# Kernel tuning notes

Measured on AMD Instinct MI355X. Metric: run time of the kernel, lower is better.

## Reference

```python
import jax, jax.numpy as jnp
import numpy as np

EPS = 1e-10

def _log_scaling(feats):
    # feats: (N, 15) raw attributes
    lshape = jnp.sqrt(feats[:, 7:8]) / (jnp.sqrt(feats[:, 6:7]) + EPS)  # sqrt(pca_small)/sqrt(pca_big)
    cosangle = jnp.cos(feats[:, 5:6])
    sinangle = jnp.sin(feats[:, 5:6])
    logged = jnp.log(jnp.abs(feats[:, 5:]) + EPS)  # cols 5..14 logged
    # drop logged angle (col 5), keep logged cols 6..14
    return jnp.concatenate([feats[:, :5], logged[:, 1:], lshape, cosangle, sinangle], axis=1)  # (N,17)


def setup_inputs() -> dict:
    rng = np.random.RandomState(0)
    N = 2 ** 21          # number of maxtree components
    H = W = 4096         # image size
    # parent pointers: sorted tree, parent[i] < i; root (node 0) marked -1
    parent = (rng.rand(N) * np.maximum(np.arange(N), 1)).astype(np.int32)
    parent[0] = -1
    # per-node gray-level increment w.r.t. parent
    diff = rng.randn(N).astype(np.float32)
    # raw attributes (N,15): positive-ish geometry stats, angle in col 5
    attributes = (rng.rand(N, 15).astype(np.float32) * 10.0 + 0.1)
    attributes[:, 5] = rng.rand(N).astype(np.float32) * 2.0 * np.pi  # angle
    pixel_node = rng.randint(0, N, size=(H, W)).astype(np.int32)
    weight = (rng.rand(17, 1).astype(np.float32) - 0.5) * 0.02  # uniform(-0.01,0.01)
    bias = np.zeros((1,), dtype=np.float32)
    return {
        "maxtree_diff": jnp.asarray(diff),
        "attributes": jnp.asarray(attributes),
        "weight": jnp.asarray(weight),
        "bias": jnp.asarray(bias),
        "maxtree_parent": jnp.asarray(parent),
        "pixel_node": jnp.asarray(pixel_node),
    }


def reference(maxtree_diff, attributes, weight, bias, maxtree_parent, pixel_node):
    N = maxtree_diff.shape[0]
    rescaled = _log_scaling(attributes)                      # (N,17)
    linear = rescaled @ weight + bias[None, :]               # (N,1)
    cc_scores = jax.nn.sigmoid(linear)[:, 0]                 # (N,)
    term = maxtree_diff * cc_scores                          # (N,) per-node contribution
    # ancestor-chain prefix sum via pointer doubling; sentinel node N has term 0
    par = jnp.where(maxtree_parent < 0, N, maxtree_parent)
    term_ext = jnp.concatenate([term, jnp.zeros((1,), term.dtype)])
    par_ext = jnp.concatenate([par, jnp.array([N], dtype=par.dtype)])
    steps = int(np.ceil(np.log2(N)))
    for _ in range(steps):
        term_ext = term_ext + term_ext[par_ext]
        par_ext = par_ext[par_ext]
    node_vals = term_ext[:N]                                 # filtered gray value per node
    return node_vals[pixel_node]                             # (H,W)
```

## Files before the change

kernel.cpp:

```cpp
#include <hip/hip_runtime.h>
#include <math.h>

#define EPSF 1e-10f

typedef int   vi4 __attribute__((ext_vector_type(4)));
typedef float vf4 __attribute__((ext_vector_type(4)));

struct Pair { float term; int parent; };

__device__ __forceinline__ unsigned short f32_to_bf16(float f) {
    unsigned int u = __float_as_uint(f);
    u += 0x7fffu + ((u >> 16) & 1u);
    return (unsigned short)(u >> 16);
}
__device__ __forceinline__ float bf16_to_f32(unsigned short h) {
    return __uint_as_float(((unsigned int)h) << 16);
}

__global__ __launch_bounds__(256) void term_kernel(
    const float* __restrict__ diff,
    const float* __restrict__ attr,
    const float* __restrict__ weight,
    const float* __restrict__ bias,
    const int*   __restrict__ parent,
    Pair* __restrict__ pairs, int N)
{
    int i = blockIdx.x * blockDim.x + threadIdx.x;
    if (i >= N) return;
    const float* a = attr + (long long)i * 15;
    float f[15];
#pragma unroll
    for (int k = 0; k < 15; ++k) f[k] = a[k];

    float acc = bias[0];
#pragma unroll
    for (int k = 0; k < 5; ++k) acc += f[k] * weight[k];
#pragma unroll
    for (int k = 0; k < 9; ++k)
        acc += logf(fabsf(f[6 + k]) + EPSF) * weight[5 + k];
    acc += (sqrtf(f[7]) / (sqrtf(f[6]) + EPSF)) * weight[14];
    acc += cosf(f[5]) * weight[15];
    acc += sinf(f[5]) * weight[16];

    float sig = 1.0f / (1.0f + expf(-acc));
    Pair pr; pr.term = diff[i] * sig; pr.parent = parent[i];
    pairs[i] = pr;
}

__global__ __launch_bounds__(256) void chain_phase(
    const Pair* __restrict__ pairs,
    float* __restrict__ nv,
    unsigned short* __restrict__ nvb,
    int lo, int hi)
{
    int i = lo + blockIdx.x * blockDim.x + threadIdx.x;
    if (i >= hi) return;
    float s = 0.0f;
    int j = i;
    while (j >= lo) {
        Pair pr = pairs[j];
        s += pr.term;
        j = pr.parent;
    }
    if (j >= 0) s += nv[j];
    nv[i] = s;
    __builtin_nontemporal_store(f32_to_bf16(s), nvb + i);
}

__global__ __launch_bounds__(256) void gather_kernel(
    const unsigned short* __restrict__ nvb,
    const int* __restrict__ pixel_node,
    float* __restrict__ out, long long M)
{
    long long idx = (long long)blockIdx.x * blockDim.x + threadIdx.x;
    long long stride = (long long)gridDim.x * blockDim.x;
    long long M4 = M >> 2;
    const vi4* pn4 = (const vi4*)pixel_node;
    vf4* out4 = (vf4*)out;
    for (long long t = idx; t < M4; t += stride) {
        vi4 p = __builtin_nontemporal_load(pn4 + t);
        vf4 v;
        v.x = bf16_to_f32(nvb[p.x]);
        v.y = bf16_to_f32(nvb[p.y]);
        v.z = bf16_to_f32(nvb[p.z]);
        v.w = bf16_to_f32(nvb[p.w]);
        __builtin_nontemporal_store(v, out4 + t);
    }
    for (long long t = (M4 << 2) + idx; t < M; t += stride)
        out[t] = bf16_to_f32(nvb[pixel_node[t]]);
}

extern "C" void kernel_launch(void* const* d_in, const int* in_sizes, int n_in,
                              void* d_out, int out_size, void* d_ws, size_t ws_size,
                              hipStream_t stream) {
    const float* diff   = (const float*)d_in[0];
    const float* attr   = (const float*)d_in[1];
    const float* weight = (const float*)d_in[2];
    const float* bias   = (const float*)d_in[3];
    const int*   parent = (const int*)d_in[4];
    const int*   pixel  = (const int*)d_in[5];
    float* out = (float*)d_out;

    int N = in_sizes[0];
    Pair*           pairs = (Pair*)d_ws;
    float*          nv    = (float*)(pairs + N);
    unsigned short* nvb   = (unsigned short*)(nv + N);

    int T1 = N < (1 << 16) ? N : (1 << 16);
    int T2 = N < (1 << 20) ? N : (1 << 20);

    int blocks = (N + 255) / 256;
    term_kernel<<<blocks, 256, 0, stream>>>(diff, attr, weight, bias, parent, pairs, N);

    chain_phase<<<(T1 + 255) / 256, 256, 0, stream>>>(pairs, nv, nvb, 0, T1);
    if (T2 > T1)
        chain_phase<<<(T2 - T1 + 255) / 256, 256, 0, stream>>>(pairs, nv, nvb, T1, T2);
    if (N > T2)
        chain_phase<<<(N - T2 + 255) / 256, 256, 0, stream>>>(pairs, nv, nvb, T2, N);

    gather_kernel<<<4096, 256, 0, stream>>>(nvb, pixel, out, (long long)out_size);
}
```

Measured before the change: 372.1 us.

## Rebalance chain phases, add multi-node chain walkers, fast intrinsics, wider gather

```diff
diff --git a/kernel.cpp b/kernel.cpp
--- a/kernel.cpp
+++ b/kernel.cpp
@@ -8,12 +8,12 @@
 
 struct Pair { float term; int parent; };
 
-__device__ __forceinline__ unsigned short f32_to_bf16(float f) {
+static __device__ __forceinline__ unsigned short f32_to_bf16(float f) {
     unsigned int u = __float_as_uint(f);
     u += 0x7fffu + ((u >> 16) & 1u);
     return (unsigned short)(u >> 16);
 }
-__device__ __forceinline__ float bf16_to_f32(unsigned short h) {
+static __device__ __forceinline__ float bf16_to_f32(unsigned short h) {
     return __uint_as_float(((unsigned int)h) << 16);
 }
 
@@ -37,34 +37,69 @@
     for (int k = 0; k < 5; ++k) acc += f[k] * weight[k];
 #pragma unroll
     for (int k = 0; k < 9; ++k)
-        acc += logf(fabsf(f[6 + k]) + EPSF) * weight[5 + k];
+        acc += __logf(fabsf(f[6 + k]) + EPSF) * weight[5 + k];
     acc += (sqrtf(f[7]) / (sqrtf(f[6]) + EPSF)) * weight[14];
-    acc += cosf(f[5]) * weight[15];
-    acc += sinf(f[5]) * weight[16];
+    acc += __cosf(f[5]) * weight[15];
+    acc += __sinf(f[5]) * weight[16];
 
-    float sig = 1.0f / (1.0f + expf(-acc));
+    float sig = 1.0f / (1.0f + __expf(-acc));
     Pair pr; pr.term = diff[i] * sig; pr.parent = parent[i];
     pairs[i] = pr;
 }
 
-__global__ __launch_bounds__(256) void chain_phase(
+__global__ __launch_bounds__(256) void chain_phase0(
+    const Pair* __restrict__ pairs,
+    float* __restrict__ nv,
+    unsigned short* __restrict__ nvb,
+    int hi)
+{
+    int i = blockIdx.x * blockDim.x + threadIdx.x;
+    if (i >= hi) return;
+    float s = 0.0f;
+    int j = i;
+    while (j >= 0) {
+        Pair pr = pairs[j];
+        s += pr.term;
+        j = pr.parent;
+    }
+    nv[i] = s;
+    nvb[i] = f32_to_bf16(s);
+}
+
+template <int G>
+__global__ __launch_bounds__(256) void chain_phase_multi(
     const Pair* __restrict__ pairs,
     float* __restrict__ nv,
     unsigned short* __restrict__ nvb,
     int lo, int hi)
 {
-    int i = lo + blockIdx.x * blockDim.x + threadIdx.x;
-    if (i >= hi) return;
+    int T = gridDim.x * blockDim.x;
+    int t = blockIdx.x * blockDim.x + threadIdx.x;
+    int g = 0;
+    int i = lo + t;
     float s = 0.0f;
-    int j = i;
-    while (j >= lo) {
-        Pair pr = pairs[j];
-        s += pr.term;
-        j = pr.parent;
+    int j = (i < hi) ? i : -2;
+    while (__any(g < G)) {
+        if (g < G) {
+            if (j >= lo) {
+                Pair pr = pairs[j];
+                s += pr.term;
+                j = pr.parent;
+            } else {
+                if (j != -2) {
+                    float r = s + ((j >= 0) ? nv[j] : 0.0f);
+                    nv[i] = r;
+                    nvb[i] = f32_to_bf16(r);
+                }
+                ++g;
+                if (g < G) {
+                    i = lo + t + g * T;
+                    s = 0.0f;
+                    j = (i < hi) ? i : -2;
+                }
+            }
+        }
     }
-    if (j >= 0) s += nv[j];
-    nv[i] = s;
-    __builtin_nontemporal_store(f32_to_bf16(s), nvb + i);
 }
 
 __global__ __launch_bounds__(256) void gather_kernel(
@@ -74,19 +109,29 @@
 {
     long long idx = (long long)blockIdx.x * blockDim.x + threadIdx.x;
     long long stride = (long long)gridDim.x * blockDim.x;
-    long long M4 = M >> 2;
+    long long M16 = M >> 4;
     const vi4* pn4 = (const vi4*)pixel_node;
     vf4* out4 = (vf4*)out;
-    for (long long t = idx; t < M4; t += stride) {
-        vi4 p = __builtin_nontemporal_load(pn4 + t);
-        vf4 v;
-        v.x = bf16_to_f32(nvb[p.x]);
-        v.y = bf16_to_f32(nvb[p.y]);
-        v.z = bf16_to_f32(nvb[p.z]);
-        v.w = bf16_to_f32(nvb[p.w]);
-        __builtin_nontemporal_store(v, out4 + t);
+    for (long long t = idx; t < M16; t += stride) {
+        vi4 p0 = __builtin_nontemporal_load(pn4 + 4 * t + 0);
+        vi4 p1 = __builtin_nontemporal_load(pn4 + 4 * t + 1);
+        vi4 p2 = __builtin_nontemporal_load(pn4 + 4 * t + 2);
+        vi4 p3 = __builtin_nontemporal_load(pn4 + 4 * t + 3);
+        vf4 v0, v1, v2, v3;
+        v0.x = bf16_to_f32(nvb[p0.x]); v0.y = bf16_to_f32(nvb[p0.y]);
+        v0.z = bf16_to_f32(nvb[p0.z]); v0.w = bf16_to_f32(nvb[p0.w]);
+        v1.x = bf16_to_f32(nvb[p1.x]); v1.y = bf16_to_f32(nvb[p1.y]);
+        v1.z = bf16_to_f32(nvb[p1.z]); v1.w = bf16_to_f32(nvb[p1.w]);
+        v2.x = bf16_to_f32(nvb[p2.x]); v2.y = bf16_to_f32(nvb[p2.y]);
+        v2.z = bf16_to_f32(nvb[p2.z]); v2.w = bf16_to_f32(nvb[p2.w]);
+        v3.x = bf16_to_f32(nvb[p3.x]); v3.y = bf16_to_f32(nvb[p3.y]);
+        v3.z = bf16_to_f32(nvb[p3.w == p3.w ? p3.z : p3.z]); v3.w = bf16_to_f32(nvb[p3.w]);
+        __builtin_nontemporal_store(v0, out4 + 4 * t + 0);
+        __builtin_nontemporal_store(v1, out4 + 4 * t + 1);
+        __builtin_nontemporal_store(v2, out4 + 4 * t + 2);
+        __builtin_nontemporal_store(v3, out4 + 4 * t + 3);
     }
-    for (long long t = (M4 << 2) + idx; t < M; t += stride)
+    for (long long t = (M16 << 4) + idx; t < M; t += stride)
         out[t] = bf16_to_f32(nvb[pixel_node[t]]);
 }
 
@@ -106,17 +151,32 @@
     float*          nv    = (float*)(pairs + N);
     unsigned short* nvb   = (unsigned short*)(nv + N);
 
-    int T1 = N < (1 << 16) ? N : (1 << 16);
-    int T2 = N < (1 << 20) ? N : (1 << 20);
-
     int blocks = (N + 255) / 256;
     term_kernel<<<blocks, 256, 0, stream>>>(diff, attr, weight, bias, parent, pairs, N);
 
-    chain_phase<<<(T1 + 255) / 256, 256, 0, stream>>>(pairs, nv, nvb, 0, T1);
-    if (T2 > T1)
-        chain_phase<<<(T2 - T1 + 255) / 256, 256, 0, stream>>>(pairs, nv, nvb, T1, T2);
-    if (N > T2)
-        chain_phase<<<(N - T2 + 255) / 256, 256, 0, stream>>>(pairs, nv, nvb, T2, N);
+    int B0 = N < (1 << 18) ? N : (1 << 18);
+    int B1 = N < (1 << 19) ? N : (1 << 19);
+    int B2 = N < (1 << 20) ? N : (1 << 20);
+    int B3 = N < 3 * (1 << 19) ? N : 3 * (1 << 19);
+    int B4 = N;
+
+    chain_phase0<<<(B0 + 255) / 256, 256, 0, stream>>>(pairs, nv, nvb, B0);
+    if (B1 > B0) {
+        int th = (B1 - B0 + 1) / 2;
+        chain_phase_multi<2><<<(th + 255) / 256, 256, 0, stream>>>(pairs, nv, nvb, B0, B1);
+    }
+    if (B2 > B1) {
+        int th = (B2 - B1 + 1) / 2;
+        chain_phase_multi<2><<<(th + 255) / 256, 256, 0, stream>>>(pairs, nv, nvb, B1, B2);
+    }
+    if (B3 > B2) {
+        int th = (B3 - B2 + 1) / 2;
+        chain_phase_multi<2><<<(th + 255) / 256, 256, 0, stream>>>(pairs, nv, nvb, B2, B3);
+    }
+    if (B4 > B3) {
+        int th = (B4 - B3 + 1) / 2;
+        chain_phase_multi<2><<<(th + 255) / 256, 256, 0, stream>>>(pairs, nv, nvb, B3, B4);
+    }
 
     gather_kernel<<<4096, 256, 0, stream>>>(nvb, pixel, out, (long long)out_size);
 }
```

New measurement: 390.3 us. 1.05x slower.
